# Kernel optimization log

Measured on AMD Instinct MI355X. Metric: run time of the kernel, lower is better.

Reference implementation:

```python
import jax, jax.numpy as jnp
import numpy as np

D_MODEL = 1024
NUM_HEADS = 16
HEAD_DIM = D_MODEL // NUM_HEADS


def setup_inputs() -> dict:
    key = jax.random.key(0)
    k_x, k_wqkv, k_bqkv, k_wfc, k_bfc = jax.random.split(key, 5)
    scale_in = 1.0 / np.sqrt(D_MODEL)
    return {
        "x": jax.random.normal(k_x, (2, 2048, D_MODEL), dtype=jnp.float32),
        # torch nn.Linear stores weight as [out_features, in_features]
        "w_qkv": jax.random.uniform(k_wqkv, (3 * D_MODEL, D_MODEL), jnp.float32, -scale_in, scale_in),
        "b_qkv": jax.random.uniform(k_bqkv, (3 * D_MODEL,), jnp.float32, -scale_in, scale_in),
        "w_fc": jax.random.uniform(k_wfc, (D_MODEL, D_MODEL), jnp.float32, -scale_in, scale_in),
        "b_fc": jax.random.uniform(k_bfc, (D_MODEL,), jnp.float32, -scale_in, scale_in),
    }


def reference(x, w_qkv, b_qkv, w_fc, b_fc):
    B, S, _ = x.shape
    # fused QKV projection: [B,S,3*d_model]
    qkv = jnp.einsum("bsd,ed->bse", x, w_qkv) + b_qkv
    # [B,S,H,3*head_dim] -> [B,H,S,3*head_dim]
    qkv = qkv.reshape(B, S, NUM_HEADS, 3 * HEAD_DIM).transpose(0, 2, 1, 3)
    Q, K, V = jnp.split(qkv, 3, axis=-1)  # each [B,H,S,head_dim]
    scores = jnp.einsum("bhqd,bhkd->bhqk", Q, K) / np.sqrt(HEAD_DIM).astype(np.float32)
    attention = jax.nn.softmax(scores, axis=-1)  # [B,H,S,S]
    values = jnp.einsum("bhqk,bhkd->bhqd", attention, V)
    # [B,H,S,head_dim] -> [B,S,d_model]
    values = values.transpose(0, 2, 1, 3).reshape(B, S, D_MODEL)
    out = jnp.einsum("bsd,ed->bse", values, w_fc) + b_fc
    return out
```

## Files before the change

### kernel.cpp

```cpp
#include <hip/hip_runtime.h>
#include <hip/hip_bf16.h>
#include <hip/hip_fp16.h>

#define D_MODEL 1024
#define NH 16
#define HD 64
#define BATCH 2
#define SEQ 2048

typedef __attribute__((ext_vector_type(8))) short short8;
typedef __attribute__((ext_vector_type(4))) float floatx4;
typedef __attribute__((ext_vector_type(16))) float floatx16;
typedef __attribute__((ext_vector_type(8))) _Float16 half8;

static __device__ __forceinline__ short f2bf(float f) {
    __hip_bfloat16 h = __float2bfloat16(f);
    return *reinterpret_cast<short*>(&h);
}
static __device__ __forceinline__ unsigned int pk2bf(float a, float b) {
    float2 t; t.x = a; t.y = b;
    __hip_bfloat162 h2 = __float22bfloat162_rn(t);
    return *reinterpret_cast<unsigned int*>(&h2);
}
static __device__ __forceinline__ void pl32swap(unsigned &a, unsigned &b) {
    asm("v_permlane32_swap_b32 %0, %1" : "+v"(a), "+v"(b));
}
static __device__ __forceinline__ short8 mk8(unsigned a, unsigned b,
                                             unsigned c, unsigned d) {
    union { unsigned u[4]; short8 s; } t;
    t.u[0] = a; t.u[1] = b; t.u[2] = c; t.u[3] = d;
    return t.s;
}

#define GLDS(gp, lp) __builtin_amdgcn_global_load_lds( \
    (const __attribute__((address_space(1))) void*)(gp), \
    (__attribute__((address_space(3))) void*)(lp), 16, 0, 0)

__global__ __launch_bounds__(256) void cvt_all(
    const float* __restrict__ x, const float* __restrict__ wq,
    const float* __restrict__ wf,
    short* __restrict__ Xb, short* __restrict__ Wqb, short* __restrict__ Wfb)
{
    int i = blockIdx.x * 256 + threadIdx.x;
    const float* src; short* dst; int off;
    if (i < 524288)      { src = x;  dst = Xb;  off = i; }
    else if (i < 917504) { src = wq; dst = Wqb; off = i - 524288; }
    else                 { src = wf; dst = Wfb; off = i - 917504; }
    float4 a = *reinterpret_cast<const float4*>(src + off * 8);
    float4 b = *reinterpret_cast<const float4*>(src + off * 8 + 4);
    short8 o;
    o[0] = f2bf(a.x); o[1] = f2bf(a.y); o[2] = f2bf(a.z); o[3] = f2bf(a.w);
    o[4] = f2bf(b.x); o[5] = f2bf(b.y); o[6] = f2bf(b.z); o[7] = f2bf(b.w);
    *reinterpret_cast<short8*>(dst + off * 8) = o;
}

__global__ __launch_bounds__(256) void qkv_gemm(
    const short* __restrict__ X, const short* __restrict__ W,
    const float* __restrict__ bias,
    short* __restrict__ Qs, short* __restrict__ Ks, short* __restrict__ Vt_g)
{
    __shared__ __align__(16) short As[128 * 128];
    __shared__ __align__(16) short Bs[128 * 128];
    const int tid = threadIdx.x;

    const int lin = blockIdx.x;
    const int g = lin & 7;
    const int loc = lin >> 3;
    const int mi = loc / 3;
    const int j3 = loc - mi * 3;
    const int m0 = mi * 128;
    const int n0 = (g + 8 * j3) * 128;
    const int bi = m0 >> 11, sl0 = m0 & 2047;

    const int w = tid >> 6, lane = tid & 63;
    const int quad = lane >> 4, l15 = lane & 15;
    const int wm2 = w >> 1, wn2 = w & 1;

    const int rg = lane >> 3;
    const int sl = lane & 7;
    const int cg = sl ^ rg;

    floatx4 acc[4][4];
#pragma unroll
    for (int i = 0; i < 4; i++)
#pragma unroll
        for (int j = 0; j < 4; j++) acc[i][j] = (floatx4)0.0f;

    for (int k0 = 0; k0 < 1024; k0 += 128) {
        __syncthreads();
#pragma unroll
        for (int jj = 0; jj < 4; jj++) {
            int grp = w * 4 + jj;
            int r = grp * 8 + rg;
#pragma unroll
            for (int kh = 0; kh < 2; kh++) {
                GLDS(&X[(size_t)(m0 + r) * 1024 + k0 + kh * 64 + cg * 8],
                     &As[grp * 1024 + kh * 512]);
                GLDS(&W[(size_t)(n0 + r) * 1024 + k0 + kh * 64 + cg * 8],
                     &Bs[grp * 1024 + kh * 512]);
            }
        }
        __syncthreads();
#pragma unroll
        for (int kk = 0; kk < 4; kk++) {
            const int kw = kk * 32 + quad * 8;
            const int base = (kw >> 6) * 512 +
                             ((((kw & 63) >> 3) ^ (l15 & 7)) * 8);
            short8 a[4], b[4];
#pragma unroll
            for (int t = 0; t < 4; t++) {
                int ra = wm2 * 64 + t * 16 + l15;
                int rb = wn2 * 64 + t * 16 + l15;
                a[t] = *reinterpret_cast<const short8*>(
                    &As[(ra >> 3) * 1024 + (ra & 7) * 64 + base]);
                b[t] = *reinterpret_cast<const short8*>(
                    &Bs[(rb >> 3) * 1024 + (rb & 7) * 64 + base]);
            }
#pragma unroll
            for (int mt = 0; mt < 4; mt++)
#pragma unroll
                for (int nt = 0; nt < 4; nt++)
                    acc[mt][nt] = __builtin_amdgcn_mfma_f32_16x16x32_bf16(
                        a[mt], b[nt], acc[mt][nt], 0, 0, 0);
        }
    }

    __syncthreads();
    short* EA = &As[0];
    short* T  = &As[0];
#pragma unroll
    for (int half = 0; half < 2; half++) {
        const int colg0 = n0 + half * 64;
        const int h = colg0 / 192;
        const int t = (colg0 % 192) / 64;
        if (wn2 == half) {
#pragma unroll
            for (int nt = 0; nt < 4; nt++) {
                int jj = nt * 16 + l15;
                float bv = bias[colg0 + jj];
#pragma unroll
                for (int mt = 0; mt < 4; mt++) {
#pragma unroll
                    for (int r = 0; r < 4; r++) {
                        int ml = wm2 * 64 + mt * 16 + quad * 4 + r;
                        float v = acc[mt][nt][r] + bv;
                        if (t == 0) v *= 0.18033688f;
                        if (t < 2) EA[ml * 72 + jj] = f2bf(v);
                        else       T[jj * 136 + ml] = f2bf(v);
                    }
                }
            }
        }
        __syncthreads();
        if (t < 2) {
            short* dst = (t == 0) ? Qs : Ks;
#pragma unroll
            for (int i = 0; i < 4; i++) {
                int c = tid + i * 256;
                int row = c >> 3, ck = c & 7;
                uint4 u = *reinterpret_cast<const uint4*>(&EA[row * 72 + ck * 8]);
                *reinterpret_cast<uint4*>(
                    &dst[((size_t)(bi * NH + h) * SEQ + sl0 + row) * HD + ck * 8]) = u;
            }
        } else {
#pragma unroll
            for (int i = 0; i < 4; i++) {
                int c = tid + i * 256;
                int d = c >> 4, ck = c & 15;
                uint4 u = *reinterpret_cast<const uint4*>(&T[d * 136 + ck * 8]);
                *reinterpret_cast<uint4*>(
                    &Vt_g[((size_t)(bi * NH + h) * HD + d) * SEQ + sl0 + ck * 8]) = u;
            }
        }
        __syncthreads();
    }
}

__global__ __launch_bounds__(256, 2) void attn_kernel(
    const short* __restrict__ Qs, const short* __restrict__ Ks,
    const short* __restrict__ Vt_g,
    _Float16* __restrict__ Opart, float* __restrict__ lpart)
{
    const int tid = threadIdx.x;
    const int w = tid >> 6, lane = tid & 63;
    const int hi = lane >> 5, l31 = lane & 31;
    const int bx = blockIdx.x;
    const int khalf = bx & 1;
    const int q0 = (bx >> 1) * 256;
    const int h = blockIdx.y, bi = blockIdx.z;
    const int bh = bi * NH + h;
    const int kbase = bh * SEQ * HD;
    const int vbase = bh * HD * SEQ;
    const int kt0 = khalf * (SEQ / 2);
    const int qw = q0 + w * 64;

    const short8 onesv = {(short)0x3F80, (short)0x3F80, (short)0x3F80, (short)0x3F80,
                          (short)0x3F80, (short)0x3F80, (short)0x3F80, (short)0x3F80};

    short8 aq[2][4];
#pragma unroll
    for (int qt = 0; qt < 2; qt++) {
        const short* qp = Qs + kbase + (size_t)(qw + qt * 32 + l31) * HD + hi * 8;
#pragma unroll
        for (int c = 0; c < 4; c++)
            aq[qt][c] = *reinterpret_cast<const short8*>(qp + c * 16);
    }

    floatx16 o[2][2], ol[2];
#pragma unroll
    for (int qt = 0; qt < 2; qt++) {
        ol[qt] = (floatx16)0.0f;
        o[qt][0] = (floatx16)0.0f;
        o[qt][1] = (floatx16)0.0f;
    }

#pragma unroll 2
    for (int it = 0; it < SEQ / 2 / 32; it++) {
        const int kt = kt0 + it * 32;
        const short* kp = Ks + kbase + (size_t)(kt + l31) * HD + hi * 8;
        short8 kf0 = *reinterpret_cast<const short8*>(kp);
        short8 kf1 = *reinterpret_cast<const short8*>(kp + 16);
        short8 kf2 = *reinterpret_cast<const short8*>(kp + 32);
        short8 kf3 = *reinterpret_cast<const short8*>(kp + 48);
        const short* vp = Vt_g + vbase + (size_t)l31 * SEQ + kt + hi * 8;
        short8 vf00 = *reinterpret_cast<const short8*>(vp);
        short8 vf10 = *reinterpret_cast<const short8*>(vp + 16);
        short8 vf01 = *reinterpret_cast<const short8*>(vp + 32 * SEQ);
        short8 vf11 = *reinterpret_cast<const short8*>(vp + 32 * SEQ + 16);

#pragma unroll
        for (int qt = 0; qt < 2; qt++) {
            floatx16 s = (floatx16)0.0f;
            s = __builtin_amdgcn_mfma_f32_32x32x16_bf16(kf0, aq[qt][0], s, 0, 0, 0);
            s = __builtin_amdgcn_mfma_f32_32x32x16_bf16(kf1, aq[qt][1], s, 0, 0, 0);
            s = __builtin_amdgcn_mfma_f32_32x32x16_bf16(kf2, aq[qt][2], s, 0, 0, 0);
            s = __builtin_amdgcn_mfma_f32_32x32x16_bf16(kf3, aq[qt][3], s, 0, 0, 0);

            float p[16];
#pragma unroll
            for (int r = 0; r < 16; r++) p[r] = exp2f(s[r]);

            unsigned d0a = pk2bf(p[0], p[1]),   d2a = pk2bf(p[4], p[5]);
            unsigned d1a = pk2bf(p[2], p[3]),   d3a = pk2bf(p[6], p[7]);
            pl32swap(d0a, d2a);
            pl32swap(d1a, d3a);
            unsigned d0b = pk2bf(p[8], p[9]),   d2b = pk2bf(p[12], p[13]);
            unsigned d1b = pk2bf(p[10], p[11]), d3b = pk2bf(p[14], p[15]);
            pl32swap(d0b, d2b);
            pl32swap(d1b, d3b);
            short8 pa0 = mk8(d0a, d1a, d2a, d3a);
            short8 pa1 = mk8(d0b, d1b, d2b, d3b);

            o[qt][0] = __builtin_amdgcn_mfma_f32_32x32x16_bf16(pa0, vf00, o[qt][0], 0, 0, 0);
            o[qt][1] = __builtin_amdgcn_mfma_f32_32x32x16_bf16(pa0, vf01, o[qt][1], 0, 0, 0);
            o[qt][0] = __builtin_amdgcn_mfma_f32_32x32x16_bf16(pa1, vf10, o[qt][0], 0, 0, 0);
            o[qt][1] = __builtin_amdgcn_mfma_f32_32x32x16_bf16(pa1, vf11, o[qt][1], 0, 0, 0);
            ol[qt] = __builtin_amdgcn_mfma_f32_32x32x16_bf16(pa0, onesv, ol[qt], 0, 0, 0);
            ol[qt] = __builtin_amdgcn_mfma_f32_32x32x16_bf16(pa1, onesv, ol[qt], 0, 0, 0);
        }
    }

#pragma unroll
    for (int qt = 0; qt < 2; qt++) {
#pragma unroll
        for (int r = 0; r < 16; r++) {
            int ql = qw + qt * 32 + (r & 3) + 8 * (r >> 2) + 4 * hi;
            size_t base = (size_t)khalf * (4096u * 1024u) +
                          ((size_t)bi * SEQ + ql) * D_MODEL + h * HD;
            Opart[base + l31]      = (_Float16)o[qt][0][r];
            Opart[base + 32 + l31] = (_Float16)o[qt][1][r];
            if (l31 == 0)
                lpart[khalf * 65536 + bh * SEQ + ql] = ol[qt][r];
        }
    }
}

__global__ __launch_bounds__(256) void combine_kernel(
    const _Float16* __restrict__ O, const float* __restrict__ lp,
    short* __restrict__ attnb)
{
    int i = blockIdx.x * 256 + threadIdx.x;
    int m = i >> 7;
    int e0 = (i & 127) * 8;
    int bi = m >> 11, s = m & 2047, h = e0 >> 6;
    int bh = bi * NH + h;
    float l = lp[bh * SEQ + s] + lp[65536 + bh * SEQ + s];
    float rl = 1.0f / l;
    size_t off = (size_t)m * D_MODEL + e0;
    half8 a = *reinterpret_cast<const half8*>(O + off);
    half8 b = *reinterpret_cast<const half8*>(O + 4096u * 1024u + off);
    short8 out;
#pragma unroll
    for (int j = 0; j < 8; j++)
        out[j] = f2bf(((float)a[j] + (float)b[j]) * rl);
    *reinterpret_cast<short8*>(attnb + off) = out;
}

__global__ __launch_bounds__(256) void fc_gemm(
    const short* __restrict__ A, const short* __restrict__ W,
    const float* __restrict__ bias, float* __restrict__ out)
{
    __shared__ __align__(16) short As[128 * 64];
    __shared__ __align__(16) short Bs[64 * 64];
    const int tid = threadIdx.x;
    const int m0 = blockIdx.y * 128;
    const int n0 = blockIdx.x * 64;
    const int w = tid >> 6, lane = tid & 63;
    const int quad = lane >> 4, l15 = lane & 15;
    const int wm2 = w >> 1, wn2 = w & 1;

    const int rg = lane >> 3;
    const int sl = lane & 7;
    const int cg = sl ^ rg;

    floatx4 acc[4][2];
#pragma unroll
    for (int i = 0; i < 4; i++)
#pragma unroll
        for (int j = 0; j < 2; j++) acc[i][j] = (floatx4)0.0f;

    for (int k0 = 0; k0 < 1024; k0 += 64) {
        __syncthreads();
#pragma unroll
        for (int j = 0; j < 4; j++) {
            int g = w * 4 + j;
            int r = g * 8 + rg;
            GLDS(&A[(size_t)(m0 + r) * 1024 + k0 + cg * 8], &As[g * 512]);
        }
#pragma unroll
        for (int j = 0; j < 2; j++) {
            int g = w * 2 + j;
            int r = g * 8 + rg;
            GLDS(&W[(size_t)(n0 + r) * 1024 + k0 + cg * 8], &Bs[g * 512]);
        }
        __syncthreads();
#pragma unroll
        for (int kk = 0; kk < 2; kk++) {
            int swz = ((kk * 4 + quad) ^ (l15 & 7)) * 8;
            short8 a[4], b[2];
#pragma unroll
            for (int i = 0; i < 4; i++)
                a[i] = *reinterpret_cast<const short8*>(
                    &As[(wm2 * 64 + i * 16 + l15) * 64 + swz]);
#pragma unroll
            for (int j = 0; j < 2; j++)
                b[j] = *reinterpret_cast<const short8*>(
                    &Bs[(wn2 * 32 + j * 16 + l15) * 64 + swz]);
#pragma unroll
            for (int mt = 0; mt < 4; mt++)
#pragma unroll
                for (int nt = 0; nt < 2; nt++)
                    acc[mt][nt] = __builtin_amdgcn_mfma_f32_16x16x32_bf16(
                        a[mt], b[nt], acc[mt][nt], 0, 0, 0);
        }
    }

#pragma unroll
    for (int nt = 0; nt < 2; nt++) {
        int col = n0 + wn2 * 32 + nt * 16 + l15;
        float bv = bias[col];
#pragma unroll
        for (int mt = 0; mt < 4; mt++) {
#pragma unroll
            for (int r = 0; r < 4; r++) {
                int row = m0 + wm2 * 64 + mt * 16 + quad * 4 + r;
                out[row * 1024 + col] = acc[mt][nt][r] + bv;
            }
        }
    }
}

extern "C" void kernel_launch(void* const* d_in, const int* in_sizes, int n_in,
                              void* d_out, int out_size, void* d_ws, size_t ws_size,
                              hipStream_t stream) {
    const float* x     = (const float*)d_in[0];
    const float* w_qkv = (const float*)d_in[1];
    const float* b_qkv = (const float*)d_in[2];
    const float* w_fc  = (const float*)d_in[3];
    const float* b_fc  = (const float*)d_in[4];
    float* out = (float*)d_out;

    const size_t M1 = 1024u * 1024u;
    short* ws = (short*)d_ws;
    short* Qs    = ws;
    short* Ks    = ws + 4 * M1;
    short* Vt_g  = ws + 8 * M1;
    short* Wfb   = ws + 12 * M1;
    short* Xb    = ws + 13 * M1;
    short* Wqb   = ws + 17 * M1;
    _Float16* Opart = (_Float16*)(ws + 13 * M1);
    float* lpart = (float*)(ws + 21 * M1);
    short* attnb = Qs;

    cvt_all<<<4096, 256, 0, stream>>>(x, w_qkv, w_fc, Xb, Wqb, Wfb);
    qkv_gemm<<<768, 256, 0, stream>>>(Xb, Wqb, b_qkv, Qs, Ks, Vt_g);
    attn_kernel<<<dim3(16, 16, 2), 256, 0, stream>>>(Qs, Ks, Vt_g, Opart, lpart);
    combine_kernel<<<2048, 256, 0, stream>>>(Opart, lpart, attnb);
    fc_gemm<<<dim3(16, 32), 256, 0, stream>>>(attnb, Wfb, b_fc, out);
}
```

Before: 218.7 us.

## Halve per-wave query tile, raise occupancy, XCD-aware block mapping, prefetch K/V

Each wave now processes one 32-query tile instead of two, cutting register pressure so launch bounds allow four blocks per CU, and the grid doubles to 1024 linear blocks. Blocks are remapped so each XCD handles whole (batch, head, key-half) groups to keep K/V in that die's L2. K and V fragments for the next iteration are loaded early to overlap memory latency with MFMA and exp work. The trade-off is that K/V global loads per query double, and the prefetch reads one tile past each key range on the final iteration.

```diff
diff --git a/kernel.cpp b/kernel.cpp
--- a/kernel.cpp
+++ b/kernel.cpp
@@ -176,7 +176,7 @@
     }
 }
 
-__global__ __launch_bounds__(256, 2) void attn_kernel(
+__global__ __launch_bounds__(256, 4) void attn_kernel(
     const short* __restrict__ Qs, const short* __restrict__ Ks,
     const short* __restrict__ Vt_g,
     _Float16* __restrict__ Opart, float* __restrict__ lpart)
@@ -184,94 +184,102 @@
     const int tid = threadIdx.x;
     const int w = tid >> 6, lane = tid & 63;
     const int hi = lane >> 5, l31 = lane & 31;
-    const int bx = blockIdx.x;
-    const int khalf = bx & 1;
-    const int q0 = (bx >> 1) * 256;
-    const int h = blockIdx.y, bi = blockIdx.z;
+
+    const int lin = blockIdx.x;
+    const int xcd = lin & 7;
+    const int j = lin >> 3;
+    const int qb = j & 15;
+    const int grp = xcd + 8 * (j >> 4);
+    const int khalf = grp & 1;
+    const int h = (grp >> 1) & 15;
+    const int bi = grp >> 5;
     const int bh = bi * NH + h;
     const int kbase = bh * SEQ * HD;
     const int vbase = bh * HD * SEQ;
     const int kt0 = khalf * (SEQ / 2);
-    const int qw = q0 + w * 64;
+    const int qw = qb * 128 + w * 32;
 
     const short8 onesv = {(short)0x3F80, (short)0x3F80, (short)0x3F80, (short)0x3F80,
                           (short)0x3F80, (short)0x3F80, (short)0x3F80, (short)0x3F80};
 
-    short8 aq[2][4];
-#pragma unroll
-    for (int qt = 0; qt < 2; qt++) {
-        const short* qp = Qs + kbase + (size_t)(qw + qt * 32 + l31) * HD + hi * 8;
+    short8 aq[4];
+    {
+        const short* qp = Qs + kbase + (size_t)(qw + l31) * HD + hi * 8;
 #pragma unroll
         for (int c = 0; c < 4; c++)
-            aq[qt][c] = *reinterpret_cast<const short8*>(qp + c * 16);
-    }
-
-    floatx16 o[2][2], ol[2];
-#pragma unroll
-    for (int qt = 0; qt < 2; qt++) {
-        ol[qt] = (floatx16)0.0f;
-        o[qt][0] = (floatx16)0.0f;
-        o[qt][1] = (floatx16)0.0f;
-    }
+            aq[c] = *reinterpret_cast<const short8*>(qp + c * 16);
+    }
+
+    floatx16 o0 = (floatx16)0.0f, o1 = (floatx16)0.0f, ol = (floatx16)0.0f;
+
+    const short* kp0 = Ks + kbase + (size_t)(kt0 + l31) * HD + hi * 8;
+    const short* vp0 = Vt_g + vbase + (size_t)l31 * SEQ + kt0 + hi * 8;
+
+    short8 kf0 = *reinterpret_cast<const short8*>(kp0);
+    short8 kf1 = *reinterpret_cast<const short8*>(kp0 + 16);
+    short8 kf2 = *reinterpret_cast<const short8*>(kp0 + 32);
+    short8 kf3 = *reinterpret_cast<const short8*>(kp0 + 48);
+    short8 vA0 = *reinterpret_cast<const short8*>(vp0);
+    short8 vA1 = *reinterpret_cast<const short8*>(vp0 + 16);
+    short8 vB0 = *reinterpret_cast<const short8*>(vp0 + 32 * SEQ);
+    short8 vB1 = *reinterpret_cast<const short8*>(vp0 + 32 * SEQ + 16);
 
 #pragma unroll 2
     for (int it = 0; it < SEQ / 2 / 32; it++) {
-        const int kt = kt0 + it * 32;
-        const short* kp = Ks + kbase + (size_t)(kt + l31) * HD + hi * 8;
-        short8 kf0 = *reinterpret_cast<const short8*>(kp);
-        short8 kf1 = *reinterpret_cast<const short8*>(kp + 16);
-        short8 kf2 = *reinterpret_cast<const short8*>(kp + 32);
-        short8 kf3 = *reinterpret_cast<const short8*>(kp + 48);
-        const short* vp = Vt_g + vbase + (size_t)l31 * SEQ + kt + hi * 8;
-        short8 vf00 = *reinterpret_cast<const short8*>(vp);
-        short8 vf10 = *reinterpret_cast<const short8*>(vp + 16);
-        short8 vf01 = *reinterpret_cast<const short8*>(vp + 32 * SEQ);
-        short8 vf11 = *reinterpret_cast<const short8*>(vp + 32 * SEQ + 16);
-
-#pragma unroll
-        for (int qt = 0; qt < 2; qt++) {
-            floatx16 s = (floatx16)0.0f;
-            s = __builtin_amdgcn_mfma_f32_32x32x16_bf16(kf0, aq[qt][0], s, 0, 0, 0);
-            s = __builtin_amdgcn_mfma_f32_32x32x16_bf16(kf1, aq[qt][1], s, 0, 0, 0);
-            s = __builtin_amdgcn_mfma_f32_32x32x16_bf16(kf2, aq[qt][2], s, 0, 0, 0);
-            s = __builtin_amdgcn_mfma_f32_32x32x16_bf16(kf3, aq[qt][3], s, 0, 0, 0);
-
-            float p[16];
-#pragma unroll
-            for (int r = 0; r < 16; r++) p[r] = exp2f(s[r]);
-
-            unsigned d0a = pk2bf(p[0], p[1]),   d2a = pk2bf(p[4], p[5]);
-            unsigned d1a = pk2bf(p[2], p[3]),   d3a = pk2bf(p[6], p[7]);
-            pl32swap(d0a, d2a);
-            pl32swap(d1a, d3a);
-            unsigned d0b = pk2bf(p[8], p[9]),   d2b = pk2bf(p[12], p[13]);
-            unsigned d1b = pk2bf(p[10], p[11]), d3b = pk2bf(p[14], p[15]);
-            pl32swap(d0b, d2b);
-            pl32swap(d1b, d3b);
-            short8 pa0 = mk8(d0a, d1a, d2a, d3a);
-            short8 pa1 = mk8(d0b, d1b, d2b, d3b);
-
-            o[qt][0] = __builtin_amdgcn_mfma_f32_32x32x16_bf16(pa0, vf00, o[qt][0], 0, 0, 0);
-            o[qt][1] = __builtin_amdgcn_mfma_f32_32x32x16_bf16(pa0, vf01, o[qt][1], 0, 0, 0);
-            o[qt][0] = __builtin_amdgcn_mfma_f32_32x32x16_bf16(pa1, vf10, o[qt][0], 0, 0, 0);
-            o[qt][1] = __builtin_amdgcn_mfma_f32_32x32x16_bf16(pa1, vf11, o[qt][1], 0, 0, 0);
-            ol[qt] = __builtin_amdgcn_mfma_f32_32x32x16_bf16(pa0, onesv, ol[qt], 0, 0, 0);
-            ol[qt] = __builtin_amdgcn_mfma_f32_32x32x16_bf16(pa1, onesv, ol[qt], 0, 0, 0);
-        }
-    }
-
-#pragma unroll
-    for (int qt = 0; qt < 2; qt++) {
-#pragma unroll
-        for (int r = 0; r < 16; r++) {
-            int ql = qw + qt * 32 + (r & 3) + 8 * (r >> 2) + 4 * hi;
-            size_t base = (size_t)khalf * (4096u * 1024u) +
-                          ((size_t)bi * SEQ + ql) * D_MODEL + h * HD;
-            Opart[base + l31]      = (_Float16)o[qt][0][r];
-            Opart[base + 32 + l31] = (_Float16)o[qt][1][r];
-            if (l31 == 0)
-                lpart[khalf * 65536 + bh * SEQ + ql] = ol[qt][r];
-        }
+        floatx16 s = (floatx16)0.0f;
+        s = __builtin_amdgcn_mfma_f32_32x32x16_bf16(kf0, aq[0], s, 0, 0, 0);
+        s = __builtin_amdgcn_mfma_f32_32x32x16_bf16(kf1, aq[1], s, 0, 0, 0);
+        s = __builtin_amdgcn_mfma_f32_32x32x16_bf16(kf2, aq[2], s, 0, 0, 0);
+        s = __builtin_amdgcn_mfma_f32_32x32x16_bf16(kf3, aq[3], s, 0, 0, 0);
+
+        {
+            const short* kpn = kp0 + (size_t)(it + 1) * (32 * HD);
+            kf0 = *reinterpret_cast<const short8*>(kpn);
+            kf1 = *reinterpret_cast<const short8*>(kpn + 16);
+            kf2 = *reinterpret_cast<const short8*>(kpn + 32);
+            kf3 = *reinterpret_cast<const short8*>(kpn + 48);
+        }
+
+        float p[16];
+#pragma unroll
+        for (int r = 0; r < 16; r++) p[r] = exp2f(s[r]);
+
+        unsigned d0a = pk2bf(p[0], p[1]),   d2a = pk2bf(p[4], p[5]);
+        unsigned d1a = pk2bf(p[2], p[3]),   d3a = pk2bf(p[6], p[7]);
+        pl32swap(d0a, d2a);
+        pl32swap(d1a, d3a);
+        unsigned d0b = pk2bf(p[8], p[9]),   d2b = pk2bf(p[12], p[13]);
+        unsigned d1b = pk2bf(p[10], p[11]), d3b = pk2bf(p[14], p[15]);
+        pl32swap(d0b, d2b);
+        pl32swap(d1b, d3b);
+        short8 pa0 = mk8(d0a, d1a, d2a, d3a);
+        short8 pa1 = mk8(d0b, d1b, d2b, d3b);
+
+        o0 = __builtin_amdgcn_mfma_f32_32x32x16_bf16(pa0, vA0, o0, 0, 0, 0);
+        o1 = __builtin_amdgcn_mfma_f32_32x32x16_bf16(pa0, vB0, o1, 0, 0, 0);
+        o0 = __builtin_amdgcn_mfma_f32_32x32x16_bf16(pa1, vA1, o0, 0, 0, 0);
+        o1 = __builtin_amdgcn_mfma_f32_32x32x16_bf16(pa1, vB1, o1, 0, 0, 0);
+        ol = __builtin_amdgcn_mfma_f32_32x32x16_bf16(pa0, onesv, ol, 0, 0, 0);
+        ol = __builtin_amdgcn_mfma_f32_32x32x16_bf16(pa1, onesv, ol, 0, 0, 0);
+
+        {
+            const short* vpn = vp0 + (it + 1) * 32;
+            vA0 = *reinterpret_cast<const short8*>(vpn);
+            vA1 = *reinterpret_cast<const short8*>(vpn + 16);
+            vB0 = *reinterpret_cast<const short8*>(vpn + 32 * SEQ);
+            vB1 = *reinterpret_cast<const short8*>(vpn + 32 * SEQ + 16);
+        }
+    }
+
+#pragma unroll
+    for (int r = 0; r < 16; r++) {
+        int ql = qw + (r & 3) + 8 * (r >> 2) + 4 * hi;
+        size_t base = (size_t)khalf * (4096u * 1024u) +
+                      ((size_t)bi * SEQ + ql) * D_MODEL + h * HD;
+        Opart[base + l31]      = (_Float16)o0[r];
+        Opart[base + 32 + l31] = (_Float16)o1[r];
+        if (l31 == 0)
+            lpart[khalf * 65536 + bh * SEQ + ql] = ol[r];
     }
 }
 
@@ -394,7 +402,7 @@
 
     cvt_all<<<4096, 256, 0, stream>>>(x, w_qkv, w_fc, Xb, Wqb, Wfb);
     qkv_gemm<<<768, 256, 0, stream>>>(Xb, Wqb, b_qkv, Qs, Ks, Vt_g);
-    attn_kernel<<<dim3(16, 16, 2), 256, 0, stream>>>(Qs, Ks, Vt_g, Opart, lpart);
+    attn_kernel<<<1024, 256, 0, stream>>>(Qs, Ks, Vt_g, Opart, lpart);
     combine_kernel<<<2048, 256, 0, stream>>>(Opart, lpart, attnb);
     fc_gemm<<<dim3(16, 32), 256, 0, stream>>>(attnb, Wfb, b_fc, out);
 }
```

Result: slower. 277.9 us (+27.0%).

## Stage K/V tiles in swizzled double-buffered LDS and remap blocks per XCD

Applied to the files above, without the earlier changes.

Before, each of the four waves in an attention block loaded the same K and V fragments straight from global memory. Now the block cooperatively copies each 32-key K/V tile into LDS with direct global-to-LDS loads, double-buffers it so the next tile is prefetched during compute, and uses an XOR swizzle to avoid bank conflicts. The grid is also flattened and remapped so that blocks sharing the same head and key half land on the same XCD, to improve L2 reuse. This adds a barrier per iteration and a prefetch past the last tile that reads into neighbouring workspace.

```diff
diff --git a/kernel.cpp b/kernel.cpp
--- a/kernel.cpp
+++ b/kernel.cpp
@@ -181,18 +181,33 @@
     const short* __restrict__ Vt_g,
     _Float16* __restrict__ Opart, float* __restrict__ lpart)
 {
+    __shared__ __align__(16) short Kl[2][32 * 64];
+    __shared__ __align__(16) short Vl[2][32 * 64];
+
     const int tid = threadIdx.x;
     const int w = tid >> 6, lane = tid & 63;
     const int hi = lane >> 5, l31 = lane & 31;
-    const int bx = blockIdx.x;
-    const int khalf = bx & 1;
-    const int q0 = (bx >> 1) * 256;
-    const int h = blockIdx.y, bi = blockIdx.z;
+
+    const int lin = blockIdx.x;
+    const int xcd = lin & 7;
+    const int j = lin >> 3;
+    const int qb = j & 7;
+    const int grp = xcd + 8 * (j >> 3);
+    const int khalf = grp & 1;
+    const int h = (grp >> 1) & 15;
+    const int bi = grp >> 5;
     const int bh = bi * NH + h;
     const int kbase = bh * SEQ * HD;
     const int vbase = bh * HD * SEQ;
     const int kt0 = khalf * (SEQ / 2);
-    const int qw = q0 + w * 64;
+    const int qw = qb * 256 + w * 64;
+
+    const int sr = tid >> 3;
+    const int ss = tid & 7;
+    const int cgs = ss ^ (sr & 7);
+    const short* kg = Ks + kbase + (size_t)(kt0 + sr) * HD + cgs * 8;
+    const short* vg = Vt_g + vbase +
+                      (size_t)(sr + (cgs >> 2) * 32) * SEQ + kt0 + (cgs & 3) * 8;
 
     const short8 onesv = {(short)0x3F80, (short)0x3F80, (short)0x3F80, (short)0x3F80,
                           (short)0x3F80, (short)0x3F80, (short)0x3F80, (short)0x3F80};
@@ -214,27 +229,37 @@
         o[qt][1] = (floatx16)0.0f;
     }
 
-#pragma unroll 2
+    const int rbase = (l31 >> 3) * 512 + (l31 & 7) * 64;
+    const int rx = l31 & 7;
+
+    GLDS(kg, &Kl[0][tid * 8]);
+    GLDS(vg, &Vl[0][tid * 8]);
+    __syncthreads();
+
+    int cur = 0;
     for (int it = 0; it < SEQ / 2 / 32; it++) {
-        const int kt = kt0 + it * 32;
-        const short* kp = Ks + kbase + (size_t)(kt + l31) * HD + hi * 8;
-        short8 kf0 = *reinterpret_cast<const short8*>(kp);
-        short8 kf1 = *reinterpret_cast<const short8*>(kp + 16);
-        short8 kf2 = *reinterpret_cast<const short8*>(kp + 32);
-        short8 kf3 = *reinterpret_cast<const short8*>(kp + 48);
-        const short* vp = Vt_g + vbase + (size_t)l31 * SEQ + kt + hi * 8;
-        short8 vf00 = *reinterpret_cast<const short8*>(vp);
-        short8 vf10 = *reinterpret_cast<const short8*>(vp + 16);
-        short8 vf01 = *reinterpret_cast<const short8*>(vp + 32 * SEQ);
-        short8 vf11 = *reinterpret_cast<const short8*>(vp + 32 * SEQ + 16);
+        GLDS(kg + (size_t)(it + 1) * (32 * HD), &Kl[cur ^ 1][tid * 8]);
+        GLDS(vg + (it + 1) * 32, &Vl[cur ^ 1][tid * 8]);
+
+        const short* Kb = &Kl[cur][0];
+        const short* Vb = &Vl[cur][0];
+        short8 kf[4], vA0, vA1, vB0, vB1;
+#pragma unroll
+        for (int c = 0; c < 4; c++)
+            kf[c] = *reinterpret_cast<const short8*>(
+                Kb + rbase + (((2 * c + hi) ^ rx) * 8));
+        vA0 = *reinterpret_cast<const short8*>(Vb + rbase + (((0 + hi) ^ rx) * 8));
+        vA1 = *reinterpret_cast<const short8*>(Vb + rbase + (((2 + hi) ^ rx) * 8));
+        vB0 = *reinterpret_cast<const short8*>(Vb + rbase + (((4 + hi) ^ rx) * 8));
+        vB1 = *reinterpret_cast<const short8*>(Vb + rbase + (((6 + hi) ^ rx) * 8));
 
 #pragma unroll
         for (int qt = 0; qt < 2; qt++) {
             floatx16 s = (floatx16)0.0f;
-            s = __builtin_amdgcn_mfma_f32_32x32x16_bf16(kf0, aq[qt][0], s, 0, 0, 0);
-            s = __builtin_amdgcn_mfma_f32_32x32x16_bf16(kf1, aq[qt][1], s, 0, 0, 0);
-            s = __builtin_amdgcn_mfma_f32_32x32x16_bf16(kf2, aq[qt][2], s, 0, 0, 0);
-            s = __builtin_amdgcn_mfma_f32_32x32x16_bf16(kf3, aq[qt][3], s, 0, 0, 0);
+            s = __builtin_amdgcn_mfma_f32_32x32x16_bf16(kf[0], aq[qt][0], s, 0, 0, 0);
+            s = __builtin_amdgcn_mfma_f32_32x32x16_bf16(kf[1], aq[qt][1], s, 0, 0, 0);
+            s = __builtin_amdgcn_mfma_f32_32x32x16_bf16(kf[2], aq[qt][2], s, 0, 0, 0);
+            s = __builtin_amdgcn_mfma_f32_32x32x16_bf16(kf[3], aq[qt][3], s, 0, 0, 0);
 
             float p[16];
 #pragma unroll
@@ -251,13 +276,16 @@
             short8 pa0 = mk8(d0a, d1a, d2a, d3a);
             short8 pa1 = mk8(d0b, d1b, d2b, d3b);
 
-            o[qt][0] = __builtin_amdgcn_mfma_f32_32x32x16_bf16(pa0, vf00, o[qt][0], 0, 0, 0);
-            o[qt][1] = __builtin_amdgcn_mfma_f32_32x32x16_bf16(pa0, vf01, o[qt][1], 0, 0, 0);
-            o[qt][0] = __builtin_amdgcn_mfma_f32_32x32x16_bf16(pa1, vf10, o[qt][0], 0, 0, 0);
-            o[qt][1] = __builtin_amdgcn_mfma_f32_32x32x16_bf16(pa1, vf11, o[qt][1], 0, 0, 0);
+            o[qt][0] = __builtin_amdgcn_mfma_f32_32x32x16_bf16(pa0, vA0, o[qt][0], 0, 0, 0);
+            o[qt][1] = __builtin_amdgcn_mfma_f32_32x32x16_bf16(pa0, vB0, o[qt][1], 0, 0, 0);
+            o[qt][0] = __builtin_amdgcn_mfma_f32_32x32x16_bf16(pa1, vA1, o[qt][0], 0, 0, 0);
+            o[qt][1] = __builtin_amdgcn_mfma_f32_32x32x16_bf16(pa1, vB1, o[qt][1], 0, 0, 0);
             ol[qt] = __builtin_amdgcn_mfma_f32_32x32x16_bf16(pa0, onesv, ol[qt], 0, 0, 0);
             ol[qt] = __builtin_amdgcn_mfma_f32_32x32x16_bf16(pa1, onesv, ol[qt], 0, 0, 0);
         }
+
+        __syncthreads();
+        cur ^= 1;
     }
 
 #pragma unroll
@@ -394,7 +422,7 @@
 
     cvt_all<<<4096, 256, 0, stream>>>(x, w_qkv, w_fc, Xb, Wqb, Wfb);
     qkv_gemm<<<768, 256, 0, stream>>>(Xb, Wqb, b_qkv, Qs, Ks, Vt_g);
-    attn_kernel<<<dim3(16, 16, 2), 256, 0, stream>>>(Qs, Ks, Vt_g, Opart, lpart);
+    attn_kernel<<<512, 256, 0, stream>>>(Qs, Ks, Vt_g, Opart, lpart);
     combine_kernel<<<2048, 256, 0, stream>>>(Opart, lpart, attnb);
     fc_gemm<<<dim3(16, 32), 256, 0, stream>>>(attnb, Wfb, b_fc, out);
 }
```

After: 214.5 us. No clear change (-2.0%).
